# Performance work log

Hardware: AMD Instinct MI355X
Metric: run time of the kernel (lower is better)

Reference implementation:

```python
import jax, jax.numpy as jnp
import numpy as np

N_NODES = 100000
N_EDGES = 1600000
IN_FEATS, HID, NUM_CLS = 128, 128, 40


def setup_inputs() -> dict:
    key = jax.random.key(0)
    ks = jax.random.split(key, 5)
    x = jax.random.normal(ks[0], (N_NODES, IN_FEATS), dtype=jnp.float32)
    # xavier-like scale for weights
    W1 = jax.random.normal(ks[1], (IN_FEATS, HID), dtype=jnp.float32) * (1.0 / np.sqrt(IN_FEATS))
    b1 = jnp.zeros((HID,), dtype=jnp.float32)
    W2 = jax.random.normal(ks[2], (HID, NUM_CLS), dtype=jnp.float32) * (1.0 / np.sqrt(HID))
    b2 = jnp.zeros((NUM_CLS,), dtype=jnp.float32)
    src = jax.random.randint(ks[3], (N_EDGES,), 0, N_NODES, dtype=jnp.int32)
    dst = jax.random.randint(ks[4], (N_EDGES,), 0, N_NODES, dtype=jnp.int32)
    return {"x": x, "W1": W1, "b1": b1, "W2": W2, "b2": b2, "src": src, "dst": dst}


def _graph_conv(h, W, b, src, dst, src_norm, dst_norm, n_nodes):
    # DGL GraphConv, norm='both': D_out^{-1/2} A D_in^{-1/2} H W + b
    # (weight-first vs aggregate-first ordering in DGL is mathematically identical)
    hs = h * src_norm[:, None]                      # [N, d] source-side norm
    msg = hs[src]                                   # [E, d] gather
    agg = jax.ops.segment_sum(msg, dst, num_segments=n_nodes)  # [N, d] scatter-add
    agg = agg * dst_norm[:, None]                   # dest-side norm
    return agg @ W + b


def reference(x, W1, b1, W2, b2, src, dst):
    n = x.shape[0]
    ones = jnp.ones(src.shape[0], dtype=x.dtype)
    out_deg = jnp.clip(jax.ops.segment_sum(ones, src, num_segments=n), 1.0)
    in_deg = jnp.clip(jax.ops.segment_sum(ones, dst, num_segments=n), 1.0)
    src_norm = out_deg ** -0.5
    dst_norm = in_deg ** -0.5
    h = jax.nn.relu(_graph_conv(x, W1, b1, src, dst, src_norm, dst_norm, n))
    return _graph_conv(h, W2, b2, src, dst, src_norm, dst_norm, n)
```

## Files before the change

### kernel.cpp

```cpp
#include <hip/hip_runtime.h>

constexpr int NN   = 100000;
constexpr int NE   = 1600000;
constexpr int INF  = 128;
constexpr int NC   = 40;

constexpr int BKSH = 9;
constexpr int NBK  = (NN + 511) / 512;
constexpr int EPB  = 4096;
constexpr int PBLK = (NE + EPB - 1) / EPB;
constexpr int CAP  = 14336;
constexpr int HB   = 391;

typedef __attribute__((ext_vector_type(8))) short short8;
typedef __attribute__((ext_vector_type(4))) float f32x4;

__device__ __forceinline__ float bflo(unsigned int u) { return __uint_as_float(u << 16); }
__device__ __forceinline__ float bfhi(unsigned int u) { return __uint_as_float(u & 0xffff0000u); }
__device__ __forceinline__ unsigned short f2bf(float f) {
    unsigned int u = __float_as_uint(f);
    return (unsigned short)((u + 0x7fffu + ((u >> 16) & 1u)) >> 16);
}
__device__ __forceinline__ unsigned int pack2(float a, float b) {
    return (unsigned int)f2bf(a) | ((unsigned int)f2bf(b) << 16);
}

__global__ __launch_bounds__(256) void histconv_kernel(const int* __restrict__ src,
                                                       const int* __restrict__ dst,
                                                       unsigned int* __restrict__ bcntD,
                                                       unsigned int* __restrict__ bcntS,
                                                       const float* __restrict__ x,
                                                       const float* __restrict__ W1,
                                                       const float* __restrict__ W2,
                                                       unsigned short* __restrict__ xh,
                                                       unsigned short* __restrict__ w1t,
                                                       unsigned short* __restrict__ w2t) {
    const int b = blockIdx.x;
    const int tid = threadIdx.x;
    if (b < HB) {
        __shared__ unsigned int hcD[NBK];
        __shared__ unsigned int hcS[NBK];
        for (int i = tid; i < NBK; i += 256) { hcD[i] = 0u; hcS[i] = 0u; }
        __syncthreads();
        int gid = b * 256 + tid;
        int stride = HB * 256;
        for (int e = gid; e < NE; e += stride) {
            atomicAdd(&hcD[dst[e] >> BKSH], 1u);
            atomicAdd(&hcS[src[e] >> BKSH], 1u);
        }
        __syncthreads();
        for (int i = tid; i < NBK; i += 256) {
            if (hcD[i]) atomicAdd(&bcntD[i], hcD[i]);
            if (hcS[i]) atomicAdd(&bcntS[i], hcS[i]);
        }
    } else if (b < HB + 6250) {
        int j = (b - HB) * 256 + tid;
        float4 v0 = ((const float4*)x)[2 * j];
        float4 v1 = ((const float4*)x)[2 * j + 1];
        uint4 o;
        o.x = pack2(v0.x, v0.y);
        o.y = pack2(v0.z, v0.w);
        o.z = pack2(v1.x, v1.y);
        o.w = pack2(v1.z, v1.w);
        ((uint4*)xh)[j] = o;
    } else if (b == HB + 6250) {
        for (int i = tid; i < 128 * 128; i += 256) {
            int k = i >> 7, n = i & 127;
            w1t[n * 128 + k] = f2bf(W1[i]);
        }
    } else {
        for (int i = tid; i < 48 * 128; i += 256) {
            int n = i >> 7, k = i & 127;
            w2t[i] = f2bf((n < NC) ? W2[k * NC + n] : 0.f);
        }
    }
}

__global__ __launch_bounds__(256) void basescan_kernel(const unsigned int* __restrict__ bcntD,
                                                       const unsigned int* __restrict__ bcntS,
                                                       int* __restrict__ baseD,
                                                       int* __restrict__ baseS) {
    __shared__ int sc[256];
    const int tid = threadIdx.x;
    int v = (tid < NBK) ? (int)bcntD[tid] : 0;
    sc[tid] = v;
    __syncthreads();
    for (int off = 1; off < 256; off <<= 1) {
        int t = (tid >= off) ? sc[tid - off] : 0;
        __syncthreads();
        sc[tid] += t;
        __syncthreads();
    }
    if (tid < NBK) baseD[tid] = sc[tid] - v;
    __syncthreads();
    v = (tid < NBK) ? (int)bcntS[tid] : 0;
    sc[tid] = v;
    __syncthreads();
    for (int off = 1; off < 256; off <<= 1) {
        int t = (tid >= off) ? sc[tid - off] : 0;
        __syncthreads();
        sc[tid] += t;
        __syncthreads();
    }
    if (tid < NBK) baseS[tid] = sc[tid] - v;
}

__global__ __launch_bounds__(256) void partition_kernel(const int* __restrict__ src,
                                                        const int* __restrict__ dst,
                                                        const int* __restrict__ baseD,
                                                        const int* __restrict__ baseS,
                                                        int* __restrict__ curD_g,
                                                        int* __restrict__ curS_g,
                                                        int* __restrict__ epartsD,
                                                        unsigned short* __restrict__ epartsS) {
    __shared__ int sc[256];
    __shared__ int cntD[NBK], gadjD[NBK], curD[NBK];
    __shared__ int cntS[NBK], gadjS[NBK], curS[NBK];
    __shared__ int stageD[EPB];
    __shared__ unsigned short stageS[EPB];
    __shared__ unsigned char bidD[EPB];
    __shared__ unsigned char bidS[EPB];
    const int tid = threadIdx.x;
    const int e0 = blockIdx.x * EPB;
    const int total = min(EPB, NE - e0);

    for (int i = tid; i < NBK; i += 256) { cntD[i] = 0; cntS[i] = 0; }
    __syncthreads();
    for (int i = tid; i < total; i += 256) {
        atomicAdd(&cntD[dst[e0 + i] >> BKSH], 1);
        atomicAdd(&cntS[src[e0 + i] >> BKSH], 1);
    }
    __syncthreads();
    {
        int v = (tid < NBK) ? cntD[tid] : 0;
        sc[tid] = v;
        __syncthreads();
        for (int off = 1; off < 256; off <<= 1) {
            int t = (tid >= off) ? sc[tid - off] : 0;
            __syncthreads();
            sc[tid] += t;
            __syncthreads();
        }
        if (tid < NBK) {
            int excl = sc[tid] - v;
            curD[tid] = excl;
            int g = (v > 0) ? atomicAdd(&curD_g[tid], v) : 0;
            gadjD[tid] = baseD[tid] + g - excl;
        }
        __syncthreads();
        v = (tid < NBK) ? cntS[tid] : 0;
        sc[tid] = v;
        __syncthreads();
        for (int off = 1; off < 256; off <<= 1) {
            int t = (tid >= off) ? sc[tid - off] : 0;
            __syncthreads();
            sc[tid] += t;
            __syncthreads();
        }
        if (tid < NBK) {
            int excl = sc[tid] - v;
            curS[tid] = excl;
            int g = (v > 0) ? atomicAdd(&curS_g[tid], v) : 0;
            gadjS[tid] = baseS[tid] + g - excl;
        }
    }
    __syncthreads();
    for (int i = tid; i < total; i += 256) {
        int s = src[e0 + i];
        int d = dst[e0 + i];
        int bD = d >> BKSH;
        int offD = atomicAdd(&curD[bD], 1);
        stageD[offD] = s | ((d - (bD << BKSH)) << 17);
        bidD[offD] = (unsigned char)bD;
        int bS = s >> BKSH;
        int offS = atomicAdd(&curS[bS], 1);
        stageS[offS] = (unsigned short)(s - (bS << BKSH));
        bidS[offS] = (unsigned char)bS;
    }
    __syncthreads();
    for (int j = tid; j < total; j += 256) {
        int b = bidD[j];
        epartsD[gadjD[b] + j] = stageD[j];
    }
    for (int j = tid; j < total; j += 256) {
        int b = bidS[j];
        epartsS[gadjS[b] + j] = stageS[j];
    }
}

__global__ __launch_bounds__(512) void pass2_kernel(const int* __restrict__ epartsD,
                                                    const unsigned short* __restrict__ epartsS,
                                                    const int* __restrict__ baseD,
                                                    const int* __restrict__ baseS_g,
                                                    const unsigned int* __restrict__ bcntD,
                                                    const unsigned int* __restrict__ bcntS,
                                                    int* __restrict__ row_ptr,
                                                    int* __restrict__ esrc,
                                                    float* __restrict__ srcn,
                                                    float* __restrict__ dstn) {
    __shared__ int hist[512];
    __shared__ int cur[512];
    __shared__ int histS[512];
    __shared__ int lesrc[CAP];
    const int tid = threadIdx.x;
    const int b = blockIdx.x;

    const int base  = baseD[b];
    const int cnt   = (int)bcntD[b];
    const int baseS = baseS_g[b];
    const int cntS  = (int)bcntS[b];
    const int n0 = b << BKSH;
    const int nloc = min(512, NN - n0);

    hist[tid] = 0;
    histS[tid] = 0;
    __syncthreads();
    for (int j = tid; j < cnt; j += 512)
        atomicAdd(&hist[epartsD[base + j] >> 17], 1);
    for (int j = tid; j < cntS; j += 512)
        atomicAdd(&histS[(int)epartsS[baseS + j]], 1);
    __syncthreads();
    int myc = hist[tid];
    int mycS = histS[tid];
    for (int off = 1; off < 512; off <<= 1) {
        int t = (tid >= off) ? hist[tid - off] : 0;
        __syncthreads();
        hist[tid] += t;
        __syncthreads();
    }
    int excl = hist[tid] - myc;
    cur[tid] = excl;
    if (tid < nloc) {
        int g = n0 + tid;
        row_ptr[g] = base + excl;
        dstn[g] = rsqrtf(fmaxf((float)myc, 1.0f));
        srcn[g] = rsqrtf(fmaxf((float)mycS, 1.0f));
    }
    if (b == NBK - 1 && tid == 0) row_ptr[NN] = NE;
    __syncthreads();
    if (cnt <= CAP) {
        for (int j = tid; j < cnt; j += 512) {
            int rec = epartsD[base + j];
            int pos = atomicAdd(&cur[rec >> 17], 1);
            lesrc[pos] = rec & 0x1FFFF;
        }
        __syncthreads();
        for (int j = tid; j < cnt; j += 512) esrc[base + j] = lesrc[j];
    } else {
        for (int j = tid; j < cnt; j += 512) {
            int rec = epartsD[base + j];
            int pos = atomicAdd(&cur[rec >> 17], 1);
            esrc[base + pos] = rec & 0x1FFFF;
        }
    }
}

__global__ __launch_bounds__(256, 4) void fused_kernel(const int* __restrict__ row_ptr,
                                                       const int* __restrict__ esrc,
                                                       const unsigned short* __restrict__ xh,
                                                       const float* __restrict__ srcn,
                                                       const unsigned short* __restrict__ w1t,
                                                       const unsigned short* __restrict__ w2t,
                                                       const float* __restrict__ b1,
                                                       const float* __restrict__ dstn,
                                                       unsigned short* __restrict__ hwb) {
    __shared__ unsigned short At[64 * 128];
    __shared__ float dn[64], sn[64], b1l[128];
    const int tid  = threadIdx.x;
    const int r0   = blockIdx.x * 64;
    const int wv   = tid >> 6;
    const int lane = tid & 63;

    if (tid < 64) {
        int r = r0 + tid;
        dn[tid] = (r < NN) ? dstn[r] : 0.f;
        sn[tid] = (r < NN) ? srcn[r] : 0.f;
    }
    if (tid >= 64 && tid < 192) b1l[tid - 64] = b1[tid - 64];
    __syncthreads();

    const int quad = lane >> 4;
    const int l16  = lane & 15;
    const int n0w  = r0 + wv * 16;
    const int rpv = row_ptr[min(n0w + min(lane, 16), NN)];

    for (int p = 0; p < 8; ++p) {
        const int begA = __shfl(rpv, 2 * p);
        const int endA = __shfl(rpv, 2 * p + 1);
        const int begB = endA;
        const int endB = __shfl(rpv, 2 * p + 2);
        float aA0 = 0.f, aA1 = 0.f, aA2 = 0.f, aA3 = 0.f;
        float aA4 = 0.f, aA5 = 0.f, aA6 = 0.f, aA7 = 0.f;
        float aB0 = 0.f, aB1 = 0.f, aB2 = 0.f, aB3 = 0.f;
        float aB4 = 0.f, aB5 = 0.f, aB6 = 0.f, aB7 = 0.f;
        for (int eA = begA, eB = begB; eA < endA || eB < endB; eA += 24, eB += 24) {
            const int remA = endA - eA;
            const int remB = endB - eB;
            int sA[6], sB[6];
#pragma unroll
            for (int t = 0; t < 6; ++t) {
                int slot = t * 4 + quad;
                sA[t] = esrc[(slot < remA) ? (eA + slot) : 0];
                sB[t] = esrc[(slot < remB) ? (eB + slot) : 0];
            }
            float nA[6], nB[6];
            uint4 uA[6], uB[6];
#pragma unroll
            for (int t = 0; t < 6; ++t) {
                int slot = t * 4 + quad;
                nA[t] = (slot < remA) ? srcn[sA[t]] : 0.f;
                nB[t] = (slot < remB) ? srcn[sB[t]] : 0.f;
                uA[t] = ((const uint4*)(xh + (size_t)sA[t] * INF))[l16];
                uB[t] = ((const uint4*)(xh + (size_t)sB[t] * INF))[l16];
            }
#pragma unroll
            for (int t = 0; t < 6; ++t) {
                aA0 += bflo(uA[t].x) * nA[t]; aA1 += bfhi(uA[t].x) * nA[t];
                aA2 += bflo(uA[t].y) * nA[t]; aA3 += bfhi(uA[t].y) * nA[t];
                aA4 += bflo(uA[t].z) * nA[t]; aA5 += bfhi(uA[t].z) * nA[t];
                aA6 += bflo(uA[t].w) * nA[t]; aA7 += bfhi(uA[t].w) * nA[t];
                aB0 += bflo(uB[t].x) * nB[t]; aB1 += bfhi(uB[t].x) * nB[t];
                aB2 += bflo(uB[t].y) * nB[t]; aB3 += bfhi(uB[t].y) * nB[t];
                aB4 += bflo(uB[t].z) * nB[t]; aB5 += bfhi(uB[t].z) * nB[t];
                aB6 += bflo(uB[t].w) * nB[t]; aB7 += bfhi(uB[t].w) * nB[t];
            }
        }
        aA0 += __shfl_down(aA0, 32); aA1 += __shfl_down(aA1, 32);
        aA2 += __shfl_down(aA2, 32); aA3 += __shfl_down(aA3, 32);
        aA4 += __shfl_down(aA4, 32); aA5 += __shfl_down(aA5, 32);
        aA6 += __shfl_down(aA6, 32); aA7 += __shfl_down(aA7, 32);
        aB0 += __shfl_down(aB0, 32); aB1 += __shfl_down(aB1, 32);
        aB2 += __shfl_down(aB2, 32); aB3 += __shfl_down(aB3, 32);
        aB4 += __shfl_down(aB4, 32); aB5 += __shfl_down(aB5, 32);
        aB6 += __shfl_down(aB6, 32); aB7 += __shfl_down(aB7, 32);
        aA0 += __shfl_down(aA0, 16); aA1 += __shfl_down(aA1, 16);
        aA2 += __shfl_down(aA2, 16); aA3 += __shfl_down(aA3, 16);
        aA4 += __shfl_down(aA4, 16); aA5 += __shfl_down(aA5, 16);
        aA6 += __shfl_down(aA6, 16); aA7 += __shfl_down(aA7, 16);
        aB0 += __shfl_down(aB0, 16); aB1 += __shfl_down(aB1, 16);
        aB2 += __shfl_down(aB2, 16); aB3 += __shfl_down(aB3, 16);
        aB4 += __shfl_down(aB4, 16); aB5 += __shfl_down(aB5, 16);
        aB6 += __shfl_down(aB6, 16); aB7 += __shfl_down(aB7, 16);
        if (lane < 16) {
            uint4 oA, oB;
            oA.x = pack2(aA0, aA1); oA.y = pack2(aA2, aA3);
            oA.z = pack2(aA4, aA5); oA.w = pack2(aA6, aA7);
            oB.x = pack2(aB0, aB1); oB.y = pack2(aB2, aB3);
            oB.z = pack2(aB4, aB5); oB.w = pack2(aB6, aB7);
            *(uint4*)&At[(wv * 16 + 2 * p) * 128 + l16 * 8] = oA;
            *(uint4*)&At[(wv * 16 + 2 * p + 1) * 128 + l16 * 8] = oB;
        }
    }

    const int lrow  = lane & 15;
    const int lquad = lane >> 4;

    short8 afrag[4];
#pragma unroll
    for (int ks = 0; ks < 4; ++ks)
        afrag[ks] = *(const short8*)&At[(wv * 16 + lrow) * 128 + ks * 32 + lquad * 8];
    float hreg[8][4];
#pragma unroll
    for (int nt = 0; nt < 8; ++nt) {
        f32x4 acc = {0.f, 0.f, 0.f, 0.f};
#pragma unroll
        for (int ks = 0; ks < 4; ++ks) {
            short8 bfr = *(const short8*)&w1t[(nt * 16 + lrow) * 128 + ks * 32 + lquad * 8];
            acc = __builtin_amdgcn_mfma_f32_16x16x32_bf16(afrag[ks], bfr, acc, 0, 0, 0);
        }
#pragma unroll
        for (int i = 0; i < 4; ++i) hreg[nt][i] = acc[i];
    }
#pragma unroll
    for (int nt = 0; nt < 8; ++nt) {
        int col = nt * 16 + lrow;
        float bb = b1l[col];
#pragma unroll
        for (int i = 0; i < 4; ++i) {
            int row = wv * 16 + lquad * 4 + i;
            At[row * 128 + col] = f2bf(fmaxf(hreg[nt][i] * dn[row] + bb, 0.f));
        }
    }

#pragma unroll
    for (int ks = 0; ks < 4; ++ks)
        afrag[ks] = *(const short8*)&At[(wv * 16 + lrow) * 128 + ks * 32 + lquad * 8];
#pragma unroll
    for (int nt = 0; nt < 3; ++nt) {
        f32x4 acc = {0.f, 0.f, 0.f, 0.f};
#pragma unroll
        for (int ks = 0; ks < 4; ++ks) {
            short8 bfr = *(const short8*)&w2t[(nt * 16 + lrow) * 128 + ks * 32 + lquad * 8];
            acc = __builtin_amdgcn_mfma_f32_16x16x32_bf16(afrag[ks], bfr, acc, 0, 0, 0);
        }
        int col = nt * 16 + lrow;
        if (col < NC) {
#pragma unroll
            for (int i = 0; i < 4; ++i) {
                int row = wv * 16 + lquad * 4 + i;
                int grow = r0 + row;
                if (grow < NN)
                    hwb[(size_t)grow * NC + col] = f2bf(acc[i] * sn[row]);
            }
        }
    }
}

__global__ __launch_bounds__(256) void gather2_kernel(const int* __restrict__ row_ptr,
                                                      const int* __restrict__ esrc,
                                                      const unsigned short* __restrict__ hwb,
                                                      const float* __restrict__ dst_norm,
                                                      const float* __restrict__ b2,
                                                      float* __restrict__ out) {
    int node = (blockIdx.x * blockDim.x + threadIdx.x) >> 6;
    int lane = threadIdx.x & 63;
    if (node >= NN) return;
    int beg = __builtin_amdgcn_readfirstlane(row_ptr[node]);
    int end = __builtin_amdgcn_readfirstlane(row_ptr[node + 1]);
    const int g = lane / 10;
    const int j = lane - g * 10;
    const bool active = (g < 6);
    float4 acc = make_float4(0.f, 0.f, 0.f, 0.f);
    for (int e = beg; e < end; e += 18) {
        const int rem = end - e;
        int s[3];
        float m[3];
#pragma unroll
        for (int q = 0; q < 3; ++q) {
            int slot = q * 6 + g;
            bool v = active && (slot < rem);
            int idx = v ? (e + slot) : beg;
            s[q] = esrc[idx];
            m[q] = v ? 1.f : 0.f;
        }
        uint2 u[3];
#pragma unroll
        for (int q = 0; q < 3; ++q)
            u[q] = ((const uint2*)(hwb + (size_t)s[q] * NC))[j];
#pragma unroll
        for (int q = 0; q < 3; ++q) {
            acc.x += bflo(u[q].x) * m[q];
            acc.y += bfhi(u[q].x) * m[q];
            acc.z += bflo(u[q].y) * m[q];
            acc.w += bfhi(u[q].y) * m[q];
        }
    }
    float4 tot = acc;
#pragma unroll
    for (int k = 1; k < 6; ++k) {
        tot.x += __shfl(acc.x, j + 10 * k);
        tot.y += __shfl(acc.y, j + 10 * k);
        tot.z += __shfl(acc.z, j + 10 * k);
        tot.w += __shfl(acc.w, j + 10 * k);
    }
    if (lane < 10) {
        float dnv = dst_norm[node];
        float4 bb = ((const float4*)b2)[j];
        float4 o;
        o.x = tot.x * dnv + bb.x;
        o.y = tot.y * dnv + bb.y;
        o.z = tot.z * dnv + bb.z;
        o.w = tot.w * dnv + bb.w;
        ((float4*)(out + (size_t)node * NC))[j] = o;
    }
}

extern "C" void kernel_launch(void* const* d_in, const int* in_sizes, int n_in,
                              void* d_out, int out_size, void* d_ws, size_t ws_size,
                              hipStream_t stream) {
    const float* x   = (const float*)d_in[0];
    const float* W1  = (const float*)d_in[1];
    const float* b1  = (const float*)d_in[2];
    const float* W2  = (const float*)d_in[3];
    const float* b2  = (const float*)d_in[4];
    const int*   src = (const int*)d_in[5];
    const int*   dst = (const int*)d_in[6];
    float* out = (float*)d_out;

    float* srcn = (float*)d_ws;
    unsigned int* bcntD = (unsigned int*)(srcn + NN);
    unsigned int* bcntS = bcntD + 256;
    int* curD  = (int*)(bcntS + 256);
    int* curS  = curD + 256;
    int* baseD = curS + 256;
    int* baseS = baseD + 256;
    int* row_ptr = baseS + 256;
    float* dstn  = (float*)(row_ptr + NN + 1);
    int* esrc    = (int*)(dstn + NN);
    size_t ofs = (size_t)NN + 1536 + (NN + 1) + NN + NE;
    ofs = (ofs + 3) & ~(size_t)3;
    unsigned short* xh   = (unsigned short*)((float*)d_ws + ofs);
    unsigned short* w1t  = xh + (size_t)NN * INF;
    unsigned short* w2t  = w1t + 128 * 128;
    unsigned short* hwb  = w2t + 48 * 128;

    int* epartsD = (int*)d_out;
    unsigned short* epartsS = (unsigned short*)(epartsD + NE);

    hipMemsetAsync(bcntD, 0, 1024 * sizeof(int), stream);

    histconv_kernel<<<HB + 6252, 256, 0, stream>>>(src, dst, bcntD, bcntS,
                                                   x, W1, W2, xh, w1t, w2t);
    basescan_kernel<<<1, 256, 0, stream>>>(bcntD, bcntS, baseD, baseS);
    partition_kernel<<<PBLK, 256, 0, stream>>>(src, dst, baseD, baseS, curD, curS,
                                               epartsD, epartsS);
    pass2_kernel<<<NBK, 512, 0, stream>>>(epartsD, epartsS, baseD, baseS,
                                          bcntD, bcntS, row_ptr, esrc, srcn, dstn);
    fused_kernel<<<(NN + 63) / 64, 256, 0, stream>>>(row_ptr, esrc, xh, srcn,
                                                     w1t, w2t, b1, dstn, hwb);
    gather2_kernel<<<(NN * 64 + 255) / 256, 256, 0, stream>>>(row_ptr, esrc, hwb,
                                                              dstn, b2, out);
}
```

Before: 307.7 us.

## Halve fused kernel row tile and split GEMM columns across wave pairs

The fused aggregation+MLP kernel now processes 32 rows per block instead of 64, so each wave aggregates 8 nodes rather than 16. For the first GEMM, pairs of waves share a 16-row tile and each computes half of the 128 output columns, and only the even waves run the second GEMM. Block barriers are added because waves now read rows written by other waves. Launch bounds rise to 8 blocks per SM and the grid doubles. The aim is lower register and LDS use per block, more blocks in flight to hide the gather latency, and less per-wave MFMA and register pressure, at the cost of extra syncs and idle waves during the second GEMM.

```diff
diff --git a/kernel.cpp b/kernel.cpp
--- a/kernel.cpp
+++ b/kernel.cpp
@@ -255,7 +255,7 @@
     }
 }
 
-__global__ __launch_bounds__(256, 4) void fused_kernel(const int* __restrict__ row_ptr,
+__global__ __launch_bounds__(256, 8) void fused_kernel(const int* __restrict__ row_ptr,
                                                        const int* __restrict__ esrc,
                                                        const unsigned short* __restrict__ xh,
                                                        const float* __restrict__ srcn,
@@ -264,14 +264,14 @@
                                                        const float* __restrict__ b1,
                                                        const float* __restrict__ dstn,
                                                        unsigned short* __restrict__ hwb) {
-    __shared__ unsigned short At[64 * 128];
-    __shared__ float dn[64], sn[64], b1l[128];
+    __shared__ unsigned short At[32 * 128];
+    __shared__ float dn[32], sn[32], b1l[128];
     const int tid  = threadIdx.x;
-    const int r0   = blockIdx.x * 64;
+    const int r0   = blockIdx.x * 32;
     const int wv   = tid >> 6;
     const int lane = tid & 63;
 
-    if (tid < 64) {
+    if (tid < 32) {
         int r = r0 + tid;
         dn[tid] = (r < NN) ? dstn[r] : 0.f;
         sn[tid] = (r < NN) ? srcn[r] : 0.f;
@@ -281,10 +281,10 @@
 
     const int quad = lane >> 4;
     const int l16  = lane & 15;
-    const int n0w  = r0 + wv * 16;
-    const int rpv = row_ptr[min(n0w + min(lane, 16), NN)];
-
-    for (int p = 0; p < 8; ++p) {
+    const int n0w  = r0 + wv * 8;
+    const int rpv = row_ptr[min(n0w + min(lane, 8), NN)];
+
+    for (int p = 0; p < 4; ++p) {
         const int begA = __shfl(rpv, 2 * p);
         const int endA = __shfl(rpv, 2 * p + 1);
         const int begB = endA;
@@ -347,60 +347,69 @@
             oA.z = pack2(aA4, aA5); oA.w = pack2(aA6, aA7);
             oB.x = pack2(aB0, aB1); oB.y = pack2(aB2, aB3);
             oB.z = pack2(aB4, aB5); oB.w = pack2(aB6, aB7);
-            *(uint4*)&At[(wv * 16 + 2 * p) * 128 + l16 * 8] = oA;
-            *(uint4*)&At[(wv * 16 + 2 * p + 1) * 128 + l16 * 8] = oB;
-        }
-    }
+            *(uint4*)&At[(wv * 8 + 2 * p) * 128 + l16 * 8] = oA;
+            *(uint4*)&At[(wv * 8 + 2 * p + 1) * 128 + l16 * 8] = oB;
+        }
+    }
+    __syncthreads();
 
     const int lrow  = lane & 15;
     const int lquad = lane >> 4;
+    const int rt    = wv >> 1;
+    const int ntB   = (wv & 1) * 4;
 
     short8 afrag[4];
 #pragma unroll
     for (int ks = 0; ks < 4; ++ks)
-        afrag[ks] = *(const short8*)&At[(wv * 16 + lrow) * 128 + ks * 32 + lquad * 8];
-    float hreg[8][4];
-#pragma unroll
-    for (int nt = 0; nt < 8; ++nt) {
+        afrag[ks] = *(const short8*)&At[(rt * 16 + lrow) * 128 + ks * 32 + lquad * 8];
+    __syncthreads();
+
+    float hreg[4][4];
+#pragma unroll
+    for (int nt2 = 0; nt2 < 4; ++nt2) {
         f32x4 acc = {0.f, 0.f, 0.f, 0.f};
 #pragma unroll
         for (int ks = 0; ks < 4; ++ks) {
-            short8 bfr = *(const short8*)&w1t[(nt * 16 + lrow) * 128 + ks * 32 + lquad * 8];
+            short8 bfr = *(const short8*)&w1t[((ntB + nt2) * 16 + lrow) * 128 + ks * 32 + lquad * 8];
             acc = __builtin_amdgcn_mfma_f32_16x16x32_bf16(afrag[ks], bfr, acc, 0, 0, 0);
         }
 #pragma unroll
-        for (int i = 0; i < 4; ++i) hreg[nt][i] = acc[i];
-    }
-#pragma unroll
-    for (int nt = 0; nt < 8; ++nt) {
-        int col = nt * 16 + lrow;
+        for (int i = 0; i < 4; ++i) hreg[nt2][i] = acc[i];
+    }
+#pragma unroll
+    for (int nt2 = 0; nt2 < 4; ++nt2) {
+        int col = (ntB + nt2) * 16 + lrow;
         float bb = b1l[col];
 #pragma unroll
         for (int i = 0; i < 4; ++i) {
-            int row = wv * 16 + lquad * 4 + i;
-            At[row * 128 + col] = f2bf(fmaxf(hreg[nt][i] * dn[row] + bb, 0.f));
-        }
-    }
-
-#pragma unroll
-    for (int ks = 0; ks < 4; ++ks)
-        afrag[ks] = *(const short8*)&At[(wv * 16 + lrow) * 128 + ks * 32 + lquad * 8];
-#pragma unroll
-    for (int nt = 0; nt < 3; ++nt) {
-        f32x4 acc = {0.f, 0.f, 0.f, 0.f};
-#pragma unroll
-        for (int ks = 0; ks < 4; ++ks) {
-            short8 bfr = *(const short8*)&w2t[(nt * 16 + lrow) * 128 + ks * 32 + lquad * 8];
-            acc = __builtin_amdgcn_mfma_f32_16x16x32_bf16(afrag[ks], bfr, acc, 0, 0, 0);
-        }
-        int col = nt * 16 + lrow;
-        if (col < NC) {
-#pragma unroll
-            for (int i = 0; i < 4; ++i) {
-                int row = wv * 16 + lquad * 4 + i;
-                int grow = r0 + row;
-                if (grow < NN)
-                    hwb[(size_t)grow * NC + col] = f2bf(acc[i] * sn[row]);
+            int row = rt * 16 + lquad * 4 + i;
+            At[row * 128 + col] = f2bf(fmaxf(hreg[nt2][i] * dn[row] + bb, 0.f));
+        }
+    }
+    __syncthreads();
+
+    if ((wv & 1) == 0) {
+        short8 hf[4];
+#pragma unroll
+        for (int ks = 0; ks < 4; ++ks)
+            hf[ks] = *(const short8*)&At[(rt * 16 + lrow) * 128 + ks * 32 + lquad * 8];
+#pragma unroll
+        for (int nt = 0; nt < 3; ++nt) {
+            f32x4 acc = {0.f, 0.f, 0.f, 0.f};
+#pragma unroll
+            for (int ks = 0; ks < 4; ++ks) {
+                short8 bfr = *(const short8*)&w2t[(nt * 16 + lrow) * 128 + ks * 32 + lquad * 8];
+                acc = __builtin_amdgcn_mfma_f32_16x16x32_bf16(hf[ks], bfr, acc, 0, 0, 0);
+            }
+            int col = nt * 16 + lrow;
+            if (col < NC) {
+#pragma unroll
+                for (int i = 0; i < 4; ++i) {
+                    int row = rt * 16 + lquad * 4 + i;
+                    int grow = r0 + row;
+                    if (grow < NN)
+                        hwb[(size_t)grow * NC + col] = f2bf(acc[i] * sn[row]);
+                }
             }
         }
     }
@@ -506,7 +515,7 @@
                                                epartsD, epartsS);
     pass2_kernel<<<NBK, 512, 0, stream>>>(epartsD, epartsS, baseD, baseS,
                                           bcntD, bcntS, row_ptr, esrc, srcn, dstn);
-    fused_kernel<<<(NN + 63) / 64, 256, 0, stream>>>(row_ptr, esrc, xh, srcn,
+    fused_kernel<<<(NN + 31) / 32, 256, 0, stream>>>(row_ptr, esrc, xh, srcn,
                                                      w1t, w2t, b1, dstn, hwb);
     gather2_kernel<<<(NN * 64 + 255) / 256, 256, 0, stream>>>(row_ptr, esrc, hwb,
                                                               dstn, b2, out);
```

Measured after the change: 463.5 us. 1.51x slower.
